# Optimization experiments

Measured on AMD Instinct MI355X. Metric: run time of the kernel, lower is better.

The kernel has to match this reference:

```python
import jax, jax.numpy as jnp
import numpy as np

N_HEADS = 8
LN_EPS = 1e-5


def _layernorm(x, g, b):
    mu = jnp.mean(x, axis=-1, keepdims=True)
    var = jnp.var(x, axis=-1, keepdims=True)
    return (x - mu) * jax.lax.rsqrt(var + LN_EPS) * g + b


def _mha(xq, xkv, W, bvec):
    # W: [4, D, D] stacked (Wq, Wk, Wv, Wo); bvec: [4, D]
    Wq, Wk, Wv, Wo = W[0], W[1], W[2], W[3]
    bq, bk, bv, bo = bvec[0], bvec[1], bvec[2], bvec[3]
    B, Lq, D = xq.shape
    Lk = xkv.shape[1]
    dh = D // N_HEADS
    q = (xq @ Wq + bq).reshape(B, Lq, N_HEADS, dh)
    k = (xkv @ Wk + bk).reshape(B, Lk, N_HEADS, dh)
    v = (xkv @ Wv + bv).reshape(B, Lk, N_HEADS, dh)
    scores = jnp.einsum('bqhd,bkhd->bhqk', q, k) / jnp.sqrt(jnp.asarray(dh, xq.dtype))
    attn = jax.nn.softmax(scores, axis=-1)
    out = jnp.einsum('bhqk,bkhd->bqhd', attn, v).reshape(B, Lq, D)
    return out @ Wo + bo


def setup_inputs() -> dict:
    key = jax.random.key(0)
    ks = jax.random.split(key, 8)
    B, A, D, F = 64, 512, 256, 512
    s = 0.02
    return {
        'trg': jax.random.normal(ks[0], (B, A, D), jnp.float32),
        'src': jax.random.normal(ks[1], (B, A, D), jnp.float32),
        'W_sa': jax.random.normal(ks[2], (4, D, D), jnp.float32) * s,
        'b_sa': jnp.zeros((4, D), jnp.float32),
        'W_ea': jax.random.normal(ks[3], (4, D, D), jnp.float32) * s,
        'b_ea': jnp.zeros((4, D), jnp.float32),
        'ln_g': jnp.ones((D,), jnp.float32),
        'ln_b': jnp.zeros((D,), jnp.float32),
        'W_fc1': jax.random.normal(ks[4], (D, F), jnp.float32) * s,
        'b_fc1': jnp.zeros((F,), jnp.float32),
        'W_fc2': jax.random.normal(ks[5], (F, F), jnp.float32) * s,
        'b_fc2': jnp.zeros((F,), jnp.float32),
        'W_out': jax.random.normal(ks[6], (F, 2), jnp.float32) * s,
        'b_out': jnp.zeros((2,), jnp.float32),
    }


def reference(trg, src, W_sa, b_sa, W_ea, b_ea, ln_g, ln_b,
              W_fc1, b_fc1, W_fc2, b_fc2, W_out, b_out):
    # n_layers = 1 decoder layer: self-attn + cross-attn, residual + LayerNorm
    h = _layernorm(trg + _mha(trg, trg, W_sa, b_sa), ln_g, ln_b)
    h = _layernorm(h + _mha(h, src, W_ea, b_ea), ln_g, ln_b)
    # norm+softmax weighted-sum pooling (fused replacement of the double loop)
    atom_norm = jnp.linalg.norm(h, axis=2)            # [B, A]
    w = jax.nn.softmax(atom_norm, axis=1)             # [B, A]
    pooled = jnp.einsum('ba,bad->bd', w, h)           # [B, D]
    # fc stack (dropout is identity in eval mode)
    h1 = jax.nn.relu(pooled @ W_fc1 + b_fc1)
    h2 = jax.nn.relu(h1 @ W_fc2 + b_fc2)
    return h2 @ W_out + b_out                          # [B, 2]
```

## Files before the change

kernel.cpp:

```cpp
#include <hip/hip_runtime.h>

typedef unsigned short u16;
typedef __attribute__((ext_vector_type(8))) short s16x8;
typedef __attribute__((ext_vector_type(8))) _Float16 f16x8;
typedef __attribute__((ext_vector_type(4))) float f32x4;

#define ASYNC16(gp, lp) \
  __builtin_amdgcn_global_load_lds((__attribute__((address_space(1))) void*)(gp), \
                                   (__attribute__((address_space(3))) void*)(lp), 16, 0, 0)

__device__ __forceinline__ u16 f2h(float f) {
  _Float16 h = (_Float16)f;
  union { _Float16 h; u16 u; } v; v.h = h;
  return v.u;
}

__device__ __forceinline__ int swz4(int row) { return (row & 3) ^ ((row >> 2) & 3); }

__global__ __launch_bounds__(256) void prep_kernel(
    const float* __restrict__ trg, const float* __restrict__ src,
    const float* __restrict__ Wsa, const float* __restrict__ Wea,
    u16* __restrict__ trg_h, u16* __restrict__ src_h, u16* __restrict__ wt)
{
  int blk = blockIdx.x, tid = threadIdx.x;
  if (blk < 8192) {
    const float* sp = (blk < 4096) ? trg : src;
    u16* dp = (blk < 4096) ? trg_h : src_h;
    size_t base = ((size_t)(blk & 4095) * 256 + tid) * 8;
    float4 a = *(const float4*)(sp + base);
    float4 c = *(const float4*)(sp + base + 4);
    s16x8 o;
    o[0] = (short)f2h(a.x); o[1] = (short)f2h(a.y);
    o[2] = (short)f2h(a.z); o[3] = (short)f2h(a.w);
    o[4] = (short)f2h(c.x); o[5] = (short)f2h(c.y);
    o[6] = (short)f2h(c.z); o[7] = (short)f2h(c.w);
    *(s16x8*)(dp + base) = o;
  } else {
    int t = (blk - 8192) * 256 + tid;
    int row = t >> 8, k = t & 255;
    const float* W; int sel, col;
    if (row < 768)       { W = Wsa; sel = row >> 8;              col = row & 255; }
    else if (row < 1024) { W = Wsa; sel = 3;                     col = row & 255; }
    else if (row < 1280) { W = Wea; sel = 0;                     col = row & 255; }
    else if (row < 1792) { W = Wea; sel = ((row - 1280) >> 8) + 1; col = (row - 1280) & 255; }
    else                 { W = Wea; sel = 3;                     col = row & 255; }
    wt[(size_t)row * 256 + k] = f2h(W[sel * 65536 + k * 256 + col]);
  }
}

__global__ __launch_bounds__(256, 3) void gemm_bias_f16(
    const u16* __restrict__ A, const u16* __restrict__ Bt,
    const float* __restrict__ bias, u16* __restrict__ C, int N)
{
  __shared__ u16 Asm[128 * 32];
  __shared__ u16 Bsm[128 * 32];
  const int tid = threadIdx.x;
  const int wv = tid >> 6, ln = tid & 63;
  const int quad = ln >> 4, l16 = ln & 15;
  const int nblk = blockIdx.x;
  const size_t arow0 = (size_t)blockIdx.y * 128;
  const size_t brow0 = (size_t)nblk * 128;
  const int wr = wv >> 1, wc = wv & 1;
  f32x4 acc[4][4];
  const f32x4 VZERO = {0.f, 0.f, 0.f, 0.f};
#pragma unroll
  for (int i = 0; i < 4; ++i)
#pragma unroll
    for (int j = 0; j < 4; ++j) acc[i][j] = VZERO;

  for (int k0 = 0; k0 < 256; k0 += 32) {
    __syncthreads();
#pragma unroll
    for (int j = 0; j < 2; ++j) {
      int c = (j * 4 + wv) * 64 + ln;
      int row = c >> 2, slot = c & 3;
      int kc = slot ^ swz4(row);
      ASYNC16(A + (arow0 + row) * 256 + k0 + kc * 8, Asm + c * 8);
      ASYNC16(Bt + (brow0 + row) * 256 + k0 + kc * 8, Bsm + c * 8);
    }
    __syncthreads();
    f16x8 af[4], bfr[4];
#pragma unroll
    for (int mt = 0; mt < 4; ++mt) {
      int tr = wr * 64 + mt * 16 + l16;
      int slot = quad ^ swz4(tr);
      af[mt] = *(const f16x8*)(Asm + (tr * 4 + slot) * 8);
    }
#pragma unroll
    for (int nt = 0; nt < 4; ++nt) {
      int tr = wc * 64 + nt * 16 + l16;
      int slot = quad ^ swz4(tr);
      bfr[nt] = *(const f16x8*)(Bsm + (tr * 4 + slot) * 8);
    }
#pragma unroll
    for (int mt = 0; mt < 4; ++mt)
#pragma unroll
      for (int nt = 0; nt < 4; ++nt)
        acc[mt][nt] = __builtin_amdgcn_mfma_f32_16x16x32_f16(af[mt], bfr[nt], acc[mt][nt], 0, 0, 0);
  }
#pragma unroll
  for (int nt = 0; nt < 4; ++nt) {
    int col = nblk * 128 + wc * 64 + nt * 16 + l16;
    float bz = bias[col];
#pragma unroll
    for (int mt = 0; mt < 4; ++mt) {
      size_t row0 = arow0 + wr * 64 + mt * 16 + quad * 4;
#pragma unroll
      for (int r = 0; r < 4; ++r)
        C[(row0 + r) * (size_t)N + col] = f2h(acc[mt][nt][r] + bz);
    }
  }
}

__global__ __launch_bounds__(256, 3) void attn_mfma(
    const u16* __restrict__ Qp, int ldq,
    const u16* __restrict__ Kp, int ldk,
    const u16* __restrict__ Vp, int ldv,
    u16* __restrict__ Op)
{
  __shared__ u16 Ks[256 * 40];
  __shared__ u16 Vt[32 * 264];
  __shared__ __align__(16) unsigned Pw[4][32 * 20];
  const int tid = threadIdx.x;
  const int wv = tid >> 6, ln = tid & 63;
  const int quad = ln >> 4, l16 = ln & 15;
  const int lin = blockIdx.x;
  const int qb = (lin >> 3) & 3;
  const int g = ((lin >> 5) << 3) | (lin & 7);
  const int h = g & 7;
  const size_t rb = (size_t)(g >> 3) * 512;
  const f32x4 VZERO = {0.f, 0.f, 0.f, 0.f};

  f16x8 qf[2];
  const _Float16 qs = (_Float16)0.25503492f;
#pragma unroll
  for (int mq = 0; mq < 2; ++mq) {
    int qrow = qb * 128 + wv * 32 + mq * 16 + l16;
    qf[mq] = *(const f16x8*)(Qp + (rb + qrow) * (size_t)ldq + h * 32 + quad * 8);
#pragma unroll
    for (int j = 0; j < 8; ++j) qf[mq][j] *= qs;
  }
  f16x8 onesf;
#pragma unroll
  for (int j = 0; j < 8; ++j) onesf[j] = (_Float16)1.0f;

  f32x4 o[2][2], osum[2];
#pragma unroll
  for (int mq = 0; mq < 2; ++mq) { o[mq][0] = VZERO; o[mq][1] = VZERO; osum[mq] = VZERO; }

  for (int kb = 0; kb < 2; ++kb) {
    __syncthreads();
    for (int c = tid; c < 1024; c += 256) {
      int row = c >> 2, part = c & 3;
      s16x8 kv = *(const s16x8*)(Kp + (rb + kb * 256 + row) * (size_t)ldk + h * 32 + part * 8);
      *(s16x8*)(Ks + row * 40 + part * 8) = kv;
      s16x8 vv = *(const s16x8*)(Vp + (rb + kb * 256 + row) * (size_t)ldv + h * 32 + part * 8);
      int kts = row >> 5, l = row & 31;
      int p = 2 * (l & 15) + (l >> 4);
#pragma unroll
      for (int j = 0; j < 8; ++j) Vt[(part * 8 + j) * 264 + kts * 32 + p] = (u16)vv[j];
    }
    __syncthreads();
    for (int kt = 0; kt < 8; ++kt) {
      f16x8 kf0 = *(const f16x8*)(Ks + (kt * 32 + l16) * 40 + quad * 8);
      f16x8 kf1 = *(const f16x8*)(Ks + (kt * 32 + 16 + l16) * 40 + quad * 8);
      f16x8 vf0 = *(const f16x8*)(Vt + l16 * 264 + kt * 32 + quad * 8);
      f16x8 vf1 = *(const f16x8*)(Vt + (16 + l16) * 264 + kt * 32 + quad * 8);
#pragma unroll
      for (int mq = 0; mq < 2; ++mq) {
        f32x4 s0 = __builtin_amdgcn_mfma_f32_16x16x32_f16(qf[mq], kf0, VZERO, 0, 0, 0);
        f32x4 s1 = __builtin_amdgcn_mfma_f32_16x16x32_f16(qf[mq], kf1, VZERO, 0, 0, 0);
#pragma unroll
        for (int r = 0; r < 4; ++r) {
          float e0 = __builtin_amdgcn_exp2f(s0[r]);
          float e1 = __builtin_amdgcn_exp2f(s1[r]);
          union { _Float16 h2[2]; unsigned u; } pk;
          pk.h2[0] = (_Float16)e0; pk.h2[1] = (_Float16)e1;
          Pw[wv][(mq * 16 + quad * 4 + r) * 20 + l16] = pk.u;
        }
      }
#pragma unroll
      for (int mq = 0; mq < 2; ++mq) {
        f16x8 pf = *(const f16x8*)(&Pw[wv][(mq * 16 + l16) * 20 + quad * 4]);
        o[mq][0] = __builtin_amdgcn_mfma_f32_16x16x32_f16(pf, vf0, o[mq][0], 0, 0, 0);
        o[mq][1] = __builtin_amdgcn_mfma_f32_16x16x32_f16(pf, vf1, o[mq][1], 0, 0, 0);
        osum[mq] = __builtin_amdgcn_mfma_f32_16x16x32_f16(pf, onesf, osum[mq], 0, 0, 0);
      }
    }
  }
#pragma unroll
  for (int mq = 0; mq < 2; ++mq)
#pragma unroll
    for (int r = 0; r < 4; ++r) {
      float inv = 1.f / osum[mq][r];
      size_t row = rb + qb * 128 + wv * 32 + mq * 16 + quad * 4 + r;
      Op[row * 256 + h * 32 + l16]      = f2h(o[mq][0][r] * inv);
      Op[row * 256 + h * 32 + 16 + l16] = f2h(o[mq][1][r] * inv);
    }
}

__global__ __launch_bounds__(256, 3) void lnproj_kernel(
    const u16* __restrict__ A, const u16* __restrict__ Wt,
    const float* __restrict__ bo, const float* resid,
    const float* __restrict__ g, const float* __restrict__ lb,
    float* Hout, u16* __restrict__ Hh, float* __restrict__ norms)
{
  __shared__ u16 Asm[64 * 32];
  __shared__ u16 Bsm[256 * 32];
  const int tid = threadIdx.x;
  const int wv = tid >> 6, ln = tid & 63;
  const int quad = ln >> 4, l16 = ln & 15;
  const size_t arow0 = (size_t)blockIdx.x * 64;
  f32x4 acc[16];
  const f32x4 VZERO = {0.f, 0.f, 0.f, 0.f};
#pragma unroll
  for (int nt = 0; nt < 16; ++nt) acc[nt] = VZERO;

  for (int k0 = 0; k0 < 256; k0 += 32) {
    __syncthreads();
    {
      int c = tid;
      int row = c >> 2, slot = c & 3;
      int kc = slot ^ swz4(row);
      ASYNC16(A + (arow0 + row) * 256 + k0 + kc * 8, Asm + c * 8);
    }
#pragma unroll
    for (int j = 0; j < 4; ++j) {
      int c = (j * 4 + wv) * 64 + ln;
      int row = c >> 2, slot = c & 3;
      int kc = slot ^ swz4(row);
      ASYNC16(Wt + (size_t)row * 256 + k0 + kc * 8, Bsm + c * 8);
    }
    __syncthreads();
    int tr = wv * 16 + l16;
    int aslot = quad ^ swz4(tr);
    f16x8 af = *(const f16x8*)(Asm + (tr * 4 + aslot) * 8);
#pragma unroll
    for (int nt = 0; nt < 16; ++nt) {
      int br = nt * 16 + l16;
      int bslot = quad ^ swz4(br);
      f16x8 bfr = *(const f16x8*)(Bsm + (br * 4 + bslot) * 8);
      acc[nt] = __builtin_amdgcn_mfma_f32_16x16x32_f16(af, bfr, acc[nt], 0, 0, 0);
    }
  }
  float gv[16], bv[16], bov[16];
#pragma unroll
  for (int nt = 0; nt < 16; ++nt) {
    int col = nt * 16 + l16;
    gv[nt] = g[col]; bv[nt] = lb[col]; bov[nt] = bo[col];
  }
#pragma unroll
  for (int r = 0; r < 4; ++r) {
    size_t row = arow0 + wv * 16 + quad * 4 + r;
    const float* rrow = resid + row * 256;
    float vals[16]; float s = 0.f;
#pragma unroll
    for (int nt = 0; nt < 16; ++nt) {
      float v = acc[nt][r] + bov[nt] + rrow[nt * 16 + l16];
      vals[nt] = v; s += v;
    }
#pragma unroll
    for (int m = 1; m < 16; m <<= 1) s += __shfl_xor(s, m);
    float mean = s * (1.f / 256.f);
    float sq = 0.f;
#pragma unroll
    for (int nt = 0; nt < 16; ++nt) { float d = vals[nt] - mean; sq = fmaf(d, d, sq); }
#pragma unroll
    for (int m = 1; m < 16; m <<= 1) sq += __shfl_xor(sq, m);
    float rstd = rsqrtf(sq * (1.f / 256.f) + 1e-5f);
    float ssq = 0.f;
    float* hrow = Hout + row * 256;
#pragma unroll
    for (int nt = 0; nt < 16; ++nt) {
      float hv = (vals[nt] - mean) * rstd * gv[nt] + bv[nt];
      hrow[nt * 16 + l16] = hv;
      if (Hh) Hh[row * 256 + nt * 16 + l16] = f2h(hv);
      ssq = fmaf(hv, hv, ssq);
    }
    if (norms) {
#pragma unroll
      for (int m = 1; m < 16; m <<= 1) ssq += __shfl_xor(ssq, m);
      if (l16 == 0) norms[row] = sqrtf(ssq);
    }
  }
}

__global__ __launch_bounds__(256) void softmax_kernel(const float* norms, float* w,
                                                      float* __restrict__ pooled)
{
  int b = blockIdx.x, tid = threadIdx.x;
  int ln = tid & 63, wvi = tid >> 6;
  __shared__ float red[8];
  const float* nb = norms + b * 512;
  float n0 = nb[tid], n1 = nb[tid + 256];
  float mx = fmaxf(n0, n1);
#pragma unroll
  for (int m = 1; m < 64; m <<= 1) mx = fmaxf(mx, __shfl_xor(mx, m));
  if (ln == 0) red[wvi] = mx;
  __syncthreads();
  mx = fmaxf(fmaxf(red[0], red[1]), fmaxf(red[2], red[3]));
  float e0 = __expf(n0 - mx), e1 = __expf(n1 - mx);
  float s = e0 + e1;
#pragma unroll
  for (int m = 1; m < 64; m <<= 1) s += __shfl_xor(s, m);
  if (ln == 0) red[4 + wvi] = s;
  __syncthreads();
  s = red[4] + red[5] + red[6] + red[7];
  float inv = 1.f / s;
  w[b * 512 + tid] = e0 * inv;
  w[b * 512 + tid + 256] = e1 * inv;
  pooled[b * 256 + tid] = 0.f;
}

__global__ __launch_bounds__(256) void poolsum_kernel(const float* __restrict__ w,
                                                      const float* __restrict__ h,
                                                      float* __restrict__ pooled)
{
  int b = blockIdx.x, sl = blockIdx.y, d = threadIdx.x;
  const float* hb = h + ((size_t)b * 512 + sl * 64) * 256 + d;
  const float* wb = w + b * 512 + sl * 64;
  float acc = 0.f;
#pragma unroll 8
  for (int a = 0; a < 64; ++a) acc = fmaf(wb[a], hb[(size_t)a * 256], acc);
  atomicAdd(&pooled[b * 256 + d], acc);
}

__global__ __launch_bounds__(512) void fc1_kernel(
    const float* __restrict__ pooled, const float* __restrict__ Wfc1,
    const float* __restrict__ bfc1, float* __restrict__ x1)
{
  int b = blockIdx.x, tid = threadIdx.x;
  __shared__ float px[256];
  if (tid < 256) px[tid] = pooled[b * 256 + tid];
  __syncthreads();
  float a = bfc1[tid];
#pragma unroll 8
  for (int d = 0; d < 256; ++d) a = fmaf(px[d], Wfc1[d * 512 + tid], a);
  x1[b * 512 + tid] = fmaxf(a, 0.f);
}

__global__ __launch_bounds__(512) void fc23_kernel(
    const float* __restrict__ x1, const float* __restrict__ Wfc2,
    const float* __restrict__ bfc2, const float* __restrict__ Wout,
    const float* __restrict__ bout, float* __restrict__ out)
{
  int b = blockIdx.x, tid = threadIdx.x;
  __shared__ float sx[512];
  __shared__ float rr[16];
  sx[tid] = x1[b * 512 + tid];
  __syncthreads();
  float a = bfc2[tid];
#pragma unroll 8
  for (int d = 0; d < 512; ++d) a = fmaf(sx[d], Wfc2[d * 512 + tid], a);
  a = fmaxf(a, 0.f);
  float p0 = a * Wout[tid * 2];
  float p1 = a * Wout[tid * 2 + 1];
  int ln = tid & 63, wvi = tid >> 6;
#pragma unroll
  for (int m = 1; m < 64; m <<= 1) { p0 += __shfl_xor(p0, m); p1 += __shfl_xor(p1, m); }
  if (ln == 0) { rr[wvi] = p0; rr[8 + wvi] = p1; }
  __syncthreads();
  if (tid == 0) {
    float s = 0.f;
#pragma unroll
    for (int i = 0; i < 8; ++i) s += rr[i];
    out[b * 2] = s + bout[0];
  }
  if (tid == 1) {
    float s = 0.f;
#pragma unroll
    for (int i = 0; i < 8; ++i) s += rr[8 + i];
    out[b * 2 + 1] = s + bout[1];
  }
}

extern "C" void kernel_launch(void* const* d_in, const int* in_sizes, int n_in,
                              void* d_out, int out_size, void* d_ws, size_t ws_size,
                              hipStream_t stream) {
  const float* trg  = (const float*)d_in[0];
  const float* src  = (const float*)d_in[1];
  const float* Wsa  = (const float*)d_in[2];
  const float* bsa  = (const float*)d_in[3];
  const float* Wea  = (const float*)d_in[4];
  const float* bea  = (const float*)d_in[5];
  const float* lng  = (const float*)d_in[6];
  const float* lnb  = (const float*)d_in[7];
  const float* Wfc1 = (const float*)d_in[8];
  const float* bfc1 = (const float*)d_in[9];
  const float* Wfc2 = (const float*)d_in[10];
  const float* bfc2 = (const float*)d_in[11];
  const float* Wout = (const float*)d_in[12];
  const float* bout = (const float*)d_in[13];
  float* out = (float*)d_out;

  const size_t M = 32768;
  char* ws = (char*)d_ws;
  u16* trg_h = (u16*)ws;                ws += M * 256 * 2;
  u16* src_h = (u16*)ws;                ws += M * 256 * 2;
  u16* wt     = (u16*)ws;               ws += 2048 * 256 * 2;
  u16* qkv    = (u16*)ws;               ws += M * 768 * 2;
  u16* attnb  = (u16*)ws;               ws += M * 256 * 2;
  float* hbuf = (float*)ws;             ws += M * 256 * 4;
  u16* hh     = (u16*)ws;               ws += M * 256 * 2;
  float* norms = (float*)ws;            ws += M * 4;
  float* pooled = (float*)ws;           ws += 64 * 256 * 4;
  float* x1buf = (float*)ws;            ws += 64 * 512 * 4;

  u16* wt_sa_qkv = wt;
  u16* wt_sa_o   = wt + 768 * 256;
  u16* wt_ea_q   = wt + 1024 * 256;
  u16* wt_ea_kv  = wt + 1280 * 256;
  u16* wt_ea_o   = wt + 1792 * 256;
  u16* kvb = qkv + M * 256;

  prep_kernel<<<10240, 256, 0, stream>>>(trg, src, Wsa, Wea, trg_h, src_h, wt);
  gemm_bias_f16<<<dim3(6, 256), 256, 0, stream>>>(trg_h, wt_sa_qkv, bsa, qkv, 768);
  attn_mfma<<<2048, 256, 0, stream>>>(qkv, 768, qkv + 256, 768, qkv + 512, 768, attnb);
  lnproj_kernel<<<512, 256, 0, stream>>>(attnb, wt_sa_o, bsa + 768, trg, lng, lnb,
                                         hbuf, hh, nullptr);
  gemm_bias_f16<<<dim3(2, 256), 256, 0, stream>>>(hh, wt_ea_q, bea, qkv, 256);
  gemm_bias_f16<<<dim3(4, 256), 256, 0, stream>>>(src_h, wt_ea_kv, bea + 256, kvb, 512);
  attn_mfma<<<2048, 256, 0, stream>>>(qkv, 256, kvb, 512, kvb + 256, 512, attnb);
  lnproj_kernel<<<512, 256, 0, stream>>>(attnb, wt_ea_o, bea + 768, hbuf, lng, lnb,
                                         hbuf, nullptr, norms);
  softmax_kernel<<<64, 256, 0, stream>>>(norms, norms, pooled);
  poolsum_kernel<<<dim3(64, 8), 256, 0, stream>>>(norms, hbuf, pooled);
  fc1_kernel<<<64, 512, 0, stream>>>(pooled, Wfc1, bfc1, x1buf);
  fc23_kernel<<<64, 512, 0, stream>>>(x1buf, Wfc2, bfc2, Wout, bout, out);

  (void)in_sizes; (void)n_in; (void)out_size; (void)ws_size;
}
```

Before: 378.7 us.

## Fuse pooling softmax and FC head into one kernel; repad V transpose in LDS

```diff
diff --git a/kernel.cpp b/kernel.cpp
--- a/kernel.cpp
+++ b/kernel.cpp
@@ -119,7 +119,7 @@
     u16* __restrict__ Op)
 {
   __shared__ u16 Ks[256 * 40];
-  __shared__ u16 Vt[32 * 264];
+  __shared__ u16 Vt[32 * 296];
   __shared__ __align__(16) unsigned Pw[4][32 * 20];
   const int tid = threadIdx.x;
   const int wv = tid >> 6, ln = tid & 63;
@@ -150,22 +150,29 @@
 
   for (int kb = 0; kb < 2; ++kb) {
     __syncthreads();
-    for (int c = tid; c < 1024; c += 256) {
-      int row = c >> 2, part = c & 3;
-      s16x8 kv = *(const s16x8*)(Kp + (rb + kb * 256 + row) * (size_t)ldk + h * 32 + part * 8);
-      *(s16x8*)(Ks + row * 40 + part * 8) = kv;
-      s16x8 vv = *(const s16x8*)(Vp + (rb + kb * 256 + row) * (size_t)ldv + h * 32 + part * 8);
-      int kts = row >> 5, l = row & 31;
-      int p = 2 * (l & 15) + (l >> 4);
-#pragma unroll
-      for (int j = 0; j < 8; ++j) Vt[(part * 8 + j) * 264 + kts * 32 + p] = (u16)vv[j];
+#pragma unroll
+    for (int it = 0; it < 4; ++it) {
+      {
+        int c = it * 256 + tid;
+        int row = c >> 2, part = c & 3;
+        s16x8 kv = *(const s16x8*)(Kp + (rb + kb * 256 + row) * (size_t)ldk + h * 32 + part * 8);
+        *(s16x8*)(Ks + row * 40 + part * 8) = kv;
+      }
+      {
+        int row = tid, part = it;
+        s16x8 vv = *(const s16x8*)(Vp + (rb + kb * 256 + row) * (size_t)ldv + h * 32 + part * 8);
+        int kts = row >> 5, l = row & 31;
+        int p = 2 * (l & 15) + (l >> 4);
+#pragma unroll
+        for (int j = 0; j < 8; ++j) Vt[(part * 8 + j) * 296 + kts * 32 + p] = (u16)vv[j];
+      }
     }
     __syncthreads();
     for (int kt = 0; kt < 8; ++kt) {
       f16x8 kf0 = *(const f16x8*)(Ks + (kt * 32 + l16) * 40 + quad * 8);
       f16x8 kf1 = *(const f16x8*)(Ks + (kt * 32 + 16 + l16) * 40 + quad * 8);
-      f16x8 vf0 = *(const f16x8*)(Vt + l16 * 264 + kt * 32 + quad * 8);
-      f16x8 vf1 = *(const f16x8*)(Vt + (16 + l16) * 264 + kt * 32 + quad * 8);
+      f16x8 vf0 = *(const f16x8*)(Vt + l16 * 296 + kt * 32 + quad * 8);
+      f16x8 vf1 = *(const f16x8*)(Vt + (16 + l16) * 296 + kt * 32 + quad * 8);
 #pragma unroll
       for (int mq = 0; mq < 2; ++mq) {
         f32x4 s0 = __builtin_amdgcn_mfma_f32_16x16x32_f16(qf[mq], kf0, VZERO, 0, 0, 0);
@@ -285,92 +292,80 @@
   }
 }
 
-__global__ __launch_bounds__(256) void softmax_kernel(const float* norms, float* w,
-                                                      float* __restrict__ pooled)
+__global__ __launch_bounds__(512) void head_kernel(
+    const float* __restrict__ norms, const float* __restrict__ h,
+    const float* __restrict__ Wfc1, const float* __restrict__ bfc1,
+    const float* __restrict__ Wfc2, const float* __restrict__ bfc2,
+    const float* __restrict__ Wout, const float* __restrict__ bout,
+    float* __restrict__ out)
 {
   int b = blockIdx.x, tid = threadIdx.x;
   int ln = tid & 63, wvi = tid >> 6;
-  __shared__ float red[8];
-  const float* nb = norms + b * 512;
-  float n0 = nb[tid], n1 = nb[tid + 256];
-  float mx = fmaxf(n0, n1);
+  __shared__ float w[512], red[16], part[512], px[256], x1[512];
+
+  float n = norms[b * 512 + tid];
+  float mx = n;
 #pragma unroll
   for (int m = 1; m < 64; m <<= 1) mx = fmaxf(mx, __shfl_xor(mx, m));
   if (ln == 0) red[wvi] = mx;
   __syncthreads();
-  mx = fmaxf(fmaxf(red[0], red[1]), fmaxf(red[2], red[3]));
-  float e0 = __expf(n0 - mx), e1 = __expf(n1 - mx);
-  float s = e0 + e1;
+  mx = red[0];
+#pragma unroll
+  for (int i = 1; i < 8; ++i) mx = fmaxf(mx, red[i]);
+  float e = __expf(n - mx);
+  float s = e;
 #pragma unroll
   for (int m = 1; m < 64; m <<= 1) s += __shfl_xor(s, m);
-  if (ln == 0) red[4 + wvi] = s;
-  __syncthreads();
-  s = red[4] + red[5] + red[6] + red[7];
-  float inv = 1.f / s;
-  w[b * 512 + tid] = e0 * inv;
-  w[b * 512 + tid + 256] = e1 * inv;
-  pooled[b * 256 + tid] = 0.f;
-}
-
-__global__ __launch_bounds__(256) void poolsum_kernel(const float* __restrict__ w,
-                                                      const float* __restrict__ h,
-                                                      float* __restrict__ pooled)
-{
-  int b = blockIdx.x, sl = blockIdx.y, d = threadIdx.x;
-  const float* hb = h + ((size_t)b * 512 + sl * 64) * 256 + d;
-  const float* wb = w + b * 512 + sl * 64;
-  float acc = 0.f;
+  if (ln == 0) red[8 + wvi] = s;
+  __syncthreads();
+  s = red[8];
+#pragma unroll
+  for (int i = 1; i < 8; ++i) s += red[8 + i];
+  w[tid] = e / s;
+  __syncthreads();
+
+  {
+    int d = tid & 255, half = tid >> 8;
+    const float* hb = h + ((size_t)b * 512 + half * 256) * 256 + d;
+    const float* wb = w + half * 256;
+    float acc = 0.f;
 #pragma unroll 8
-  for (int a = 0; a < 64; ++a) acc = fmaf(wb[a], hb[(size_t)a * 256], acc);
-  atomicAdd(&pooled[b * 256 + d], acc);
-}
-
-__global__ __launch_bounds__(512) void fc1_kernel(
-    const float* __restrict__ pooled, const float* __restrict__ Wfc1,
-    const float* __restrict__ bfc1, float* __restrict__ x1)
-{
-  int b = blockIdx.x, tid = threadIdx.x;
-  __shared__ float px[256];
-  if (tid < 256) px[tid] = pooled[b * 256 + tid];
-  __syncthreads();
-  float a = bfc1[tid];
+    for (int a = 0; a < 256; ++a) acc = fmaf(wb[a], hb[(size_t)a * 256], acc);
+    part[tid] = acc;
+  }
+  __syncthreads();
+  if (tid < 256) px[tid] = part[tid] + part[tid + 256];
+  __syncthreads();
+
+  {
+    float a = bfc1[tid];
 #pragma unroll 8
-  for (int d = 0; d < 256; ++d) a = fmaf(px[d], Wfc1[d * 512 + tid], a);
-  x1[b * 512 + tid] = fmaxf(a, 0.f);
-}
-
-__global__ __launch_bounds__(512) void fc23_kernel(
-    const float* __restrict__ x1, const float* __restrict__ Wfc2,
-    const float* __restrict__ bfc2, const float* __restrict__ Wout,
-    const float* __restrict__ bout, float* __restrict__ out)
-{
-  int b = blockIdx.x, tid = threadIdx.x;
-  __shared__ float sx[512];
-  __shared__ float rr[16];
-  sx[tid] = x1[b * 512 + tid];
-  __syncthreads();
+    for (int d = 0; d < 256; ++d) a = fmaf(px[d], Wfc1[d * 512 + tid], a);
+    x1[tid] = fmaxf(a, 0.f);
+  }
+  __syncthreads();
+
   float a = bfc2[tid];
 #pragma unroll 8
-  for (int d = 0; d < 512; ++d) a = fmaf(sx[d], Wfc2[d * 512 + tid], a);
+  for (int d = 0; d < 512; ++d) a = fmaf(x1[d], Wfc2[d * 512 + tid], a);
   a = fmaxf(a, 0.f);
   float p0 = a * Wout[tid * 2];
   float p1 = a * Wout[tid * 2 + 1];
-  int ln = tid & 63, wvi = tid >> 6;
 #pragma unroll
   for (int m = 1; m < 64; m <<= 1) { p0 += __shfl_xor(p0, m); p1 += __shfl_xor(p1, m); }
-  if (ln == 0) { rr[wvi] = p0; rr[8 + wvi] = p1; }
+  if (ln == 0) { red[wvi] = p0; red[8 + wvi] = p1; }
   __syncthreads();
   if (tid == 0) {
-    float s = 0.f;
-#pragma unroll
-    for (int i = 0; i < 8; ++i) s += rr[i];
-    out[b * 2] = s + bout[0];
+    float t = 0.f;
+#pragma unroll
+    for (int i = 0; i < 8; ++i) t += red[i];
+    out[b * 2] = t + bout[0];
   }
   if (tid == 1) {
-    float s = 0.f;
-#pragma unroll
-    for (int i = 0; i < 8; ++i) s += rr[8 + i];
-    out[b * 2 + 1] = s + bout[1];
+    float t = 0.f;
+#pragma unroll
+    for (int i = 0; i < 8; ++i) t += red[8 + i];
+    out[b * 2 + 1] = t + bout[1];
   }
 }
 
@@ -403,8 +398,6 @@
   float* hbuf = (float*)ws;             ws += M * 256 * 4;
   u16* hh     = (u16*)ws;               ws += M * 256 * 2;
   float* norms = (float*)ws;            ws += M * 4;
-  float* pooled = (float*)ws;           ws += 64 * 256 * 4;
-  float* x1buf = (float*)ws;            ws += 64 * 512 * 4;
 
   u16* wt_sa_qkv = wt;
   u16* wt_sa_o   = wt + 768 * 256;
@@ -423,10 +416,8 @@
   attn_mfma<<<2048, 256, 0, stream>>>(qkv, 256, kvb, 512, kvb + 256, 512, attnb);
   lnproj_kernel<<<512, 256, 0, stream>>>(attnb, wt_ea_o, bea + 768, hbuf, lng, lnb,
                                          hbuf, nullptr, norms);
-  softmax_kernel<<<64, 256, 0, stream>>>(norms, norms, pooled);
-  poolsum_kernel<<<dim3(64, 8), 256, 0, stream>>>(norms, hbuf, pooled);
-  fc1_kernel<<<64, 512, 0, stream>>>(pooled, Wfc1, bfc1, x1buf);
-  fc23_kernel<<<64, 512, 0, stream>>>(x1buf, Wfc2, bfc2, Wout, bout, out);
+  head_kernel<<<64, 512, 0, stream>>>(norms, hbuf, Wfc1, bfc1, Wfc2, bfc2,
+                                      Wout, bout, out);
 
   (void)in_sizes; (void)n_in; (void)out_size; (void)ws_size;
 }
```

Result: slower. 390.2 us (+3.1%).

## Keep residual hidden state in fp16 and restage V transpose loads

Applied to the files above, without the earlier changes.

```diff
diff --git a/kernel.cpp b/kernel.cpp
--- a/kernel.cpp
+++ b/kernel.cpp
@@ -13,6 +13,9 @@
   _Float16 h = (_Float16)f;
   union { _Float16 h; u16 u; } v; v.h = h;
   return v.u;
+}
+__device__ __forceinline__ float h2f(u16 s) {
+  union { _Float16 h; u16 u; } v; v.u = s; return (float)v.h;
 }
 
 __device__ __forceinline__ int swz4(int row) { return (row & 3) ^ ((row >> 2) & 3); }
@@ -119,7 +122,7 @@
     u16* __restrict__ Op)
 {
   __shared__ u16 Ks[256 * 40];
-  __shared__ u16 Vt[32 * 264];
+  __shared__ u16 Vt[32 * 296];
   __shared__ __align__(16) unsigned Pw[4][32 * 20];
   const int tid = threadIdx.x;
   const int wv = tid >> 6, ln = tid & 63;
@@ -150,22 +153,29 @@
 
   for (int kb = 0; kb < 2; ++kb) {
     __syncthreads();
-    for (int c = tid; c < 1024; c += 256) {
-      int row = c >> 2, part = c & 3;
-      s16x8 kv = *(const s16x8*)(Kp + (rb + kb * 256 + row) * (size_t)ldk + h * 32 + part * 8);
-      *(s16x8*)(Ks + row * 40 + part * 8) = kv;
-      s16x8 vv = *(const s16x8*)(Vp + (rb + kb * 256 + row) * (size_t)ldv + h * 32 + part * 8);
-      int kts = row >> 5, l = row & 31;
-      int p = 2 * (l & 15) + (l >> 4);
-#pragma unroll
-      for (int j = 0; j < 8; ++j) Vt[(part * 8 + j) * 264 + kts * 32 + p] = (u16)vv[j];
+#pragma unroll
+    for (int it = 0; it < 4; ++it) {
+      {
+        int c = it * 256 + tid;
+        int row = c >> 2, part = c & 3;
+        s16x8 kv = *(const s16x8*)(Kp + (rb + kb * 256 + row) * (size_t)ldk + h * 32 + part * 8);
+        *(s16x8*)(Ks + row * 40 + part * 8) = kv;
+      }
+      {
+        int row = tid, part = it;
+        s16x8 vv = *(const s16x8*)(Vp + (rb + kb * 256 + row) * (size_t)ldv + h * 32 + part * 8);
+        int kts = row >> 5, l = row & 31;
+        int p = 2 * (l & 15) + (l >> 4);
+#pragma unroll
+        for (int j = 0; j < 8; ++j) Vt[(part * 8 + j) * 296 + kts * 32 + p] = (u16)vv[j];
+      }
     }
     __syncthreads();
     for (int kt = 0; kt < 8; ++kt) {
       f16x8 kf0 = *(const f16x8*)(Ks + (kt * 32 + l16) * 40 + quad * 8);
       f16x8 kf1 = *(const f16x8*)(Ks + (kt * 32 + 16 + l16) * 40 + quad * 8);
-      f16x8 vf0 = *(const f16x8*)(Vt + l16 * 264 + kt * 32 + quad * 8);
-      f16x8 vf1 = *(const f16x8*)(Vt + (16 + l16) * 264 + kt * 32 + quad * 8);
+      f16x8 vf0 = *(const f16x8*)(Vt + l16 * 296 + kt * 32 + quad * 8);
+      f16x8 vf1 = *(const f16x8*)(Vt + (16 + l16) * 296 + kt * 32 + quad * 8);
 #pragma unroll
       for (int mq = 0; mq < 2; ++mq) {
         f32x4 s0 = __builtin_amdgcn_mfma_f32_16x16x32_f16(qf[mq], kf0, VZERO, 0, 0, 0);
@@ -201,9 +211,9 @@
 
 __global__ __launch_bounds__(256, 3) void lnproj_kernel(
     const u16* __restrict__ A, const u16* __restrict__ Wt,
-    const float* __restrict__ bo, const float* resid,
+    const float* __restrict__ bo, const u16* __restrict__ resid,
     const float* __restrict__ g, const float* __restrict__ lb,
-    float* Hout, u16* __restrict__ Hh, float* __restrict__ norms)
+    u16* __restrict__ Hh, float* __restrict__ norms)
 {
   __shared__ u16 Asm[64 * 32];
   __shared__ u16 Bsm[256 * 32];
@@ -252,11 +262,11 @@
 #pragma unroll
   for (int r = 0; r < 4; ++r) {
     size_t row = arow0 + wv * 16 + quad * 4 + r;
-    const float* rrow = resid + row * 256;
+    const u16* rrow = resid + row * 256;
     float vals[16]; float s = 0.f;
 #pragma unroll
     for (int nt = 0; nt < 16; ++nt) {
-      float v = acc[nt][r] + bov[nt] + rrow[nt * 16 + l16];
+      float v = acc[nt][r] + bov[nt] + h2f(rrow[nt * 16 + l16]);
       vals[nt] = v; s += v;
     }
 #pragma unroll
@@ -269,12 +279,10 @@
     for (int m = 1; m < 16; m <<= 1) sq += __shfl_xor(sq, m);
     float rstd = rsqrtf(sq * (1.f / 256.f) + 1e-5f);
     float ssq = 0.f;
-    float* hrow = Hout + row * 256;
 #pragma unroll
     for (int nt = 0; nt < 16; ++nt) {
       float hv = (vals[nt] - mean) * rstd * gv[nt] + bv[nt];
-      hrow[nt * 16 + l16] = hv;
-      if (Hh) Hh[row * 256 + nt * 16 + l16] = f2h(hv);
+      Hh[row * 256 + nt * 16 + l16] = f2h(hv);
       ssq = fmaf(hv, hv, ssq);
     }
     if (norms) {
@@ -313,15 +321,15 @@
 }
 
 __global__ __launch_bounds__(256) void poolsum_kernel(const float* __restrict__ w,
-                                                      const float* __restrict__ h,
+                                                      const u16* __restrict__ h,
                                                       float* __restrict__ pooled)
 {
   int b = blockIdx.x, sl = blockIdx.y, d = threadIdx.x;
-  const float* hb = h + ((size_t)b * 512 + sl * 64) * 256 + d;
+  const u16* hb = h + ((size_t)b * 512 + sl * 64) * 256 + d;
   const float* wb = w + b * 512 + sl * 64;
   float acc = 0.f;
 #pragma unroll 8
-  for (int a = 0; a < 64; ++a) acc = fmaf(wb[a], hb[(size_t)a * 256], acc);
+  for (int a = 0; a < 64; ++a) acc = fmaf(wb[a], h2f(hb[(size_t)a * 256]), acc);
   atomicAdd(&pooled[b * 256 + d], acc);
 }
 
@@ -400,8 +408,8 @@
   u16* wt     = (u16*)ws;               ws += 2048 * 256 * 2;
   u16* qkv    = (u16*)ws;               ws += M * 768 * 2;
   u16* attnb  = (u16*)ws;               ws += M * 256 * 2;
-  float* hbuf = (float*)ws;             ws += M * 256 * 4;
   u16* hh     = (u16*)ws;               ws += M * 256 * 2;
+  u16* h2h    = (u16*)ws;               ws += M * 256 * 2;
   float* norms = (float*)ws;            ws += M * 4;
   float* pooled = (float*)ws;           ws += 64 * 256 * 4;
   float* x1buf = (float*)ws;            ws += 64 * 512 * 4;
@@ -416,15 +424,15 @@
   prep_kernel<<<10240, 256, 0, stream>>>(trg, src, Wsa, Wea, trg_h, src_h, wt);
   gemm_bias_f16<<<dim3(6, 256), 256, 0, stream>>>(trg_h, wt_sa_qkv, bsa, qkv, 768);
   attn_mfma<<<2048, 256, 0, stream>>>(qkv, 768, qkv + 256, 768, qkv + 512, 768, attnb);
-  lnproj_kernel<<<512, 256, 0, stream>>>(attnb, wt_sa_o, bsa + 768, trg, lng, lnb,
-                                         hbuf, hh, nullptr);
+  lnproj_kernel<<<512, 256, 0, stream>>>(attnb, wt_sa_o, bsa + 768, trg_h, lng, lnb,
+                                         hh, nullptr);
   gemm_bias_f16<<<dim3(2, 256), 256, 0, stream>>>(hh, wt_ea_q, bea, qkv, 256);
   gemm_bias_f16<<<dim3(4, 256), 256, 0, stream>>>(src_h, wt_ea_kv, bea + 256, kvb, 512);
   attn_mfma<<<2048, 256, 0, stream>>>(qkv, 256, kvb, 512, kvb + 256, 512, attnb);
-  lnproj_kernel<<<512, 256, 0, stream>>>(attnb, wt_ea_o, bea + 768, hbuf, lng, lnb,
-                                         hbuf, nullptr, norms);
+  lnproj_kernel<<<512, 256, 0, stream>>>(attnb, wt_ea_o, bea + 768, hh, lng, lnb,
+                                         h2h, norms);
   softmax_kernel<<<64, 256, 0, stream>>>(norms, norms, pooled);
-  poolsum_kernel<<<dim3(64, 8), 256, 0, stream>>>(norms, hbuf, pooled);
+  poolsum_kernel<<<dim3(64, 8), 256, 0, stream>>>(norms, h2h, pooled);
   fc1_kernel<<<64, 512, 0, stream>>>(pooled, Wfc1, bfc1, x1buf);
   fc23_kernel<<<64, 512, 0, stream>>>(x1buf, Wfc2, bfc2, Wout, bout, out);
 
```

Measured after the change: 354.6 us. -6.4%, faster.
